# Kernel tuning notes

Hardware: AMD Instinct MI355X
Metric: run time of the kernel (lower is better)

The kernel has to match this reference:

```python
import jax, jax.numpy as jnp
import numpy as np

B, N_GLOBAL, D, E = 4096, 64, 256, 4
TPE = N_GLOBAL // E
EPS = 1e-5


def setup_inputs() -> dict:
    key = jax.random.key(0)
    ks = jax.random.split(key, 5)
    X_global = jax.random.normal(ks[0], (B, N_GLOBAL, D), dtype=jnp.float32)
    # per-expert deep MLP params: Linear(tpe*d -> d), Linear(d -> tpe*d)
    f = TPE * D
    W1 = jax.random.normal(ks[1], (E, f, D), dtype=jnp.float32) * (f ** -0.5)
    b1 = jax.random.normal(ks[2], (E, D), dtype=jnp.float32) * 0.01
    W2 = jax.random.normal(ks[3], (E, D, f), dtype=jnp.float32) * (D ** -0.5)
    b2 = jax.random.normal(ks[4], (E, f), dtype=jnp.float32) * 0.01
    gamma = jnp.ones((E, D), dtype=jnp.float32)
    beta = jnp.zeros((E, D), dtype=jnp.float32)
    return {"X_global": X_global, "W1": W1, "b1": b1, "W2": W2, "b2": b2,
            "gamma": gamma, "beta": beta}


def reference(X_global, W1, b1, W2, b2, gamma, beta):
    Bn, n_global, d = X_global.shape
    e = W1.shape[0]
    tpe = n_global // e
    scale = d ** -0.5
    # static partition: (B, E, tpe, d)
    Xp = X_global.reshape(Bn, e, tpe, d)
    # DOT-product self-attention per expert partition
    scores = jnp.einsum('bend,bemd->benm', Xp, Xp) * scale  # (B,E,tpe,tpe)
    X_dot = jnp.einsum('benm,bemd->bend', jax.nn.softmax(scores, axis=-1), Xp)
    # deep MLP on flattened partition
    Xf = Xp.reshape(Bn, e, tpe * d)
    h = jax.nn.relu(jnp.einsum('bef,efh->beh', Xf, W1) + b1[None])  # (B,E,d)
    X_deep = (jnp.einsum('beh,ehf->bef', h, W2) + b2[None]).reshape(Bn, e, tpe, d)
    # residual + LayerNorm over last dim (biased variance, eps=1e-5)
    Y = X_dot + X_deep + Xp
    mu = jnp.mean(Y, axis=-1, keepdims=True)
    var = jnp.mean(jnp.square(Y - mu), axis=-1, keepdims=True)
    Yn = (Y - mu) * jax.lax.rsqrt(var + EPS)
    Yn = Yn * gamma[None, :, None, :] + beta[None, :, None, :]
    return Yn.reshape(Bn, n_global, d)
```

## Files before the change

kernel.cpp:

```cpp
#include <hip/hip_runtime.h>


typedef __attribute__((ext_vector_type(4))) float f32x4;
typedef __bf16 bf16;
typedef __attribute__((ext_vector_type(8))) bf16 bf16x8;

#define DEV static __device__ __forceinline__

DEV f32x4 zero4() { return f32x4{0.f, 0.f, 0.f, 0.f}; }

DEV bf16x8 cvt8(const f32x4& a, const f32x4& b) {
  bf16x8 o;
  o[0] = (bf16)a.x; o[1] = (bf16)a.y; o[2] = (bf16)a.z; o[3] = (bf16)a.w;
  o[4] = (bf16)b.x; o[5] = (bf16)b.y; o[6] = (bf16)b.z; o[7] = (bf16)b.w;
  return o;
}

__global__ __launch_bounds__(256) void pack_w1(const float* __restrict__ W1,
                                               bf16* __restrict__ P) {
  const int e = blockIdx.z, kc = blockIdx.y;
  const int nf = blockIdx.x * 4 + (threadIdx.x >> 6);
  const int l = threadIdx.x & 63;
  const float* src = W1 + (size_t)e * 4096 * 256 +
                     (size_t)(kc * 32 + (l >> 4) * 8) * 256 + nf * 16 + (l & 15);
  bf16x8 o;
#pragma unroll
  for (int j = 0; j < 8; j++) o[j] = (bf16)src[(size_t)j * 256];
  *(bf16x8*)&P[(((size_t)e * 128 + kc) * 16 + nf) * 512 + l * 8] = o;
}

__global__ __launch_bounds__(256) void pack_w2(const float* __restrict__ W2,
                                               bf16* __restrict__ P) {
  const int e = blockIdx.z, t = blockIdx.y, kc = blockIdx.x;
  const int l = threadIdx.x & 63;
#pragma unroll
  for (int it = 0; it < 4; it++) {
    int nfl = it * 4 + (threadIdx.x >> 6);
    const float* src = W2 + (size_t)e * 256 * 4096 +
                       (size_t)(kc * 32 + (l >> 4) * 8) * 4096 + t * 256 +
                       nfl * 16 + (l & 15);
    bf16x8 o;
#pragma unroll
    for (int j = 0; j < 8; j++) o[j] = (bf16)src[(size_t)j * 4096];
    *(bf16x8*)&P[(((size_t)e * 256 + t * 16 + nfl) * 8 + kc) * 512 + l * 8] = o;
  }
}

__global__ __launch_bounds__(256) void fused_ag(
    const float* __restrict__ X, const bf16* __restrict__ W1P,
    const float* __restrict__ b1, float* __restrict__ Y0f,
    bf16* __restrict__ Y0b, bf16* __restrict__ HP, int useBf) {
  __shared__ __align__(16) bf16 S[4 * 4224];
  __shared__ __align__(16) bf16 Pl[4 * 512];
  const int tid = threadIdx.x, lane = tid & 63, w = tid >> 6;
  const int lr = lane & 15, g = lane >> 4;
  const int fid = blockIdx.x;
  const int e = (fid & 7) >> 1;
  const int m = ((fid >> 3) << 1) | (fid & 1);
  const int b0 = m * 32;

  {
    bf16* xt = &S[w * 4224];
    bf16* pl = &Pl[w * 512];
    for (int q = lane; q < 256; q += 64) {
      int row = q >> 4, cc = q & 15;
      pl[row * 32 + 16 + cc] = (bf16)0.f;
    }

    for (int q = 0; q < 8; q++) {
      const int bp = b0 + q * 4 + w;
      const size_t obase0 = (size_t)bp * 16384 + e * 4096;
      const float* Xb = X + obase0;

      xt[4096 + lane] = (bf16)0.f;

      bf16x8 af[8];
#pragma unroll
      for (int c = 0; c < 8; c++) {
        const float* qq = Xb + lr * 256 + c * 32 + g * 8;
        f32x4 v0 = *(const f32x4*)qq;
        f32x4 v1 = *(const f32x4*)(qq + 4);
        bf16x8 o = cvt8(v0, v1);
        af[c] = o;
#pragma unroll
        for (int j = 0; j < 8; j++)
          xt[(c * 32 + g * 8 + j) * 16 + lr] = o[j];
      }

      f32x4 s = zero4();
#pragma unroll
      for (int c = 0; c < 8; c++)
        s = __builtin_amdgcn_mfma_f32_16x16x32_bf16(af[c], af[c], s, 0, 0, 0);

      float pv[4];
#pragma unroll
      for (int r = 0; r < 4; r++) {
        float v = s[r] * 0.0625f;
        float mx = v;
#pragma unroll
        for (int mm = 1; mm < 16; mm <<= 1) mx = fmaxf(mx, __shfl_xor(mx, mm));
        float ev = __expf(v - mx);
        float sum = ev;
#pragma unroll
        for (int mm = 1; mm < 16; mm <<= 1) sum += __shfl_xor(sum, mm);
        pv[r] = ev / sum;
      }
#pragma unroll
      for (int r = 0; r < 4; r++) pl[(g * 4 + r) * 32 + lr] = (bf16)pv[r];
      bf16x8 pf = *(const bf16x8*)&pl[lr * 32 + g * 8];

      float yo[16][4];
#pragma unroll
      for (int nc = 0; nc < 16; nc++) {
        bf16x8 bfr = *(const bf16x8*)&xt[(nc * 16 + lr) * 16 + g * 8];
        f32x4 xd =
            __builtin_amdgcn_mfma_f32_16x16x32_bf16(pf, bfr, zero4(), 0, 0, 0);
#pragma unroll
        for (int r = 0; r < 4; r++)
          yo[nc][r] = xd[r] + (float)xt[(nc * 16 + lr) * 16 + g * 4 + r];
      }

#pragma unroll
      for (int nc = 0; nc < 16; nc++)
#pragma unroll
        for (int r = 0; r < 4; r++)
          xt[(g * 4 + r) * 264 + nc * 16 + lr] = (bf16)yo[nc][r];

      const int tok = lane >> 2, cc = lane & 3;
      if (useBf) {
#pragma unroll
        for (int i = 0; i < 8; i++) {
          int d0 = i * 32 + cc * 8;
          bf16x8 v = *(const bf16x8*)&xt[tok * 264 + d0];
          *(bf16x8*)&Y0b[obase0 + tok * 256 + d0] = v;
        }
      } else {
#pragma unroll
        for (int i = 0; i < 8; i++) {
          int d0 = i * 32 + cc * 8;
          bf16x8 v = *(const bf16x8*)&xt[tok * 264 + d0];
          f32x4 a, bb;
          a.x = (float)v[0]; a.y = (float)v[1];
          a.z = (float)v[2]; a.w = (float)v[3];
          bb.x = (float)v[4]; bb.y = (float)v[5];
          bb.z = (float)v[6]; bb.w = (float)v[7];
          *(f32x4*)&Y0f[obase0 + tok * 256 + d0] = a;
          *(f32x4*)&Y0f[obase0 + tok * 256 + d0 + 4] = bb;
        }
      }
    }
  }
  __syncthreads();

  {
    bf16* Ab0 = S;
    bf16* Ab1 = S + 4352;
    const int arow = tid >> 3, ak0 = (tid & 7) * 16;
    const size_t abase = (size_t)(b0 + arow) * 16384 + e * 4096 + ak0;
    const bf16* Wp = W1P + (size_t)e * 128 * 16 * 512;

    f32x4 acc[2][4];
#pragma unroll
    for (int i = 0; i < 2; i++)
#pragma unroll
      for (int j = 0; j < 4; j++) acc[i][j] = zero4();

    f32x4 p0, p1, p2, p3;
    {
      const float* q = X + abase;
      p0 = *(const f32x4*)q;       p1 = *(const f32x4*)(q + 4);
      p2 = *(const f32x4*)(q + 8); p3 = *(const f32x4*)(q + 12);
    }

    for (int kt = 0; kt < 32; kt++) {
      bf16* Ac = (kt & 1) ? Ab1 : Ab0;
      *(bf16x8*)&Ac[arow * 136 + ak0] = cvt8(p0, p1);
      *(bf16x8*)&Ac[arow * 136 + ak0 + 8] = cvt8(p2, p3);
      if (kt < 31) {
        const float* q = X + abase + (kt + 1) * 128;
        p0 = *(const f32x4*)q;       p1 = *(const f32x4*)(q + 4);
        p2 = *(const f32x4*)(q + 8); p3 = *(const f32x4*)(q + 12);
      }
      __syncthreads();
#pragma unroll
      for (int kki = 0; kki < 4; kki++) {
        const int kc = kt * 4 + kki;
        bf16x8 afr[2], bfr[4];
#pragma unroll
        for (int i = 0; i < 2; i++)
          afr[i] = *(const bf16x8*)&Ac[(i * 16 + lr) * 136 + kki * 32 + g * 8];
#pragma unroll
        for (int j = 0; j < 4; j++)
          bfr[j] = *(const bf16x8*)&Wp[(((size_t)kc) * 16 + w * 4 + j) * 512 +
                                       lane * 8];
#pragma unroll
        for (int i = 0; i < 2; i++)
#pragma unroll
          for (int j = 0; j < 4; j++)
            acc[i][j] = __builtin_amdgcn_mfma_f32_16x16x32_bf16(
                afr[i], bfr[j], acc[i][j], 0, 0, 0);
      }
      __syncthreads();
    }
#pragma unroll
    for (int j = 0; j < 4; j++) {
      const int col = w * 64 + j * 16 + lr;
      const float bv = b1[e * 256 + col];
      const int kc = col >> 5, lhi = (col >> 3) & 3, jj = col & 7;
#pragma unroll
      for (int i = 0; i < 2; i++) {
        const int mfg = m * 2 + i;
        bf16* dst = HP + (((size_t)e * 256 + mfg) * 8 + kc) * 512 + jj;
#pragma unroll
        for (int r = 0; r < 4; r++) {
          float v = fmaxf(acc[i][j][r] + bv, 0.f);
          dst[(lhi * 16 + g * 4 + r) * 8] = (bf16)v;
        }
      }
    }
  }
}

__global__ __launch_bounds__(512) void gemm2_kernel(
    const bf16* __restrict__ HP, const bf16* __restrict__ W2P,
    const float* __restrict__ b2, const float* __restrict__ gamma,
    const float* __restrict__ beta, const float* __restrict__ Y0f,
    const bf16* __restrict__ Y0b, int useBf, float* __restrict__ Out) {
  __shared__ __align__(16) bf16 T[64 * 264];
  const int fid = blockIdx.x;
  const int e = fid & 3;
  const int rr_ = fid >> 2;
  const int t = rr_ & 15;
  const int ms = rr_ >> 4;
  const int tid = threadIdx.x, lane = tid & 63, w = tid >> 6;
  const int lr = lane & 15, g = lane >> 4;
  const int erow = tid >> 3, ec = tid & 7;

  bf16x8 breg[2][8];
  {
    const bf16* Wp = W2P + (((size_t)e * 256 + t * 16 + w * 2) * 8) * 512 +
                     lane * 8;
#pragma unroll
    for (int nj = 0; nj < 2; nj++)
#pragma unroll
      for (int kc = 0; kc < 8; kc++)
        breg[nj][kc] = *(const bf16x8*)&Wp[(size_t)(nj * 8 + kc) * 512];
  }
  float b2v[2];
#pragma unroll
  for (int nj = 0; nj < 2; nj++)
    b2v[nj] = b2[e * 4096 + t * 256 + w * 32 + nj * 16 + lr];

  for (int it = 0; it < 2; it++) {
    const int mt = ms * 2 + it;
    const int b0 = mt * 64;
    const size_t ebase =
        (size_t)(b0 + erow) * 16384 + e * 4096 + t * 256 + ec * 32;

    bf16x8 y0r[4];
    if (useBf) {
#pragma unroll
      for (int u = 0; u < 4; u++)
        y0r[u] = *(const bf16x8*)&Y0b[ebase + u * 8];
    }

    const bf16* Ap = HP + (((size_t)e * 256 + mt * 4) * 8) * 512 + lane * 8;
    f32x4 acc[4][2];
#pragma unroll
    for (int mf = 0; mf < 4; mf++)
#pragma unroll
      for (int nj = 0; nj < 2; nj++) acc[mf][nj] = zero4();

    bf16x8 afr[4], afn[4];
#pragma unroll
    for (int mf = 0; mf < 4; mf++)
      afr[mf] = *(const bf16x8*)&Ap[(size_t)(mf * 8) * 512];
#pragma unroll
    for (int kc = 0; kc < 8; kc++) {
      if (kc < 7) {
#pragma unroll
        for (int mf = 0; mf < 4; mf++)
          afn[mf] = *(const bf16x8*)&Ap[(size_t)(mf * 8 + kc + 1) * 512];
      }
#pragma unroll
      for (int mf = 0; mf < 4; mf++)
#pragma unroll
        for (int nj = 0; nj < 2; nj++)
          acc[mf][nj] = __builtin_amdgcn_mfma_f32_16x16x32_bf16(
              afr[mf], breg[nj][kc], acc[mf][nj], 0, 0, 0);
#pragma unroll
      for (int mf = 0; mf < 4; mf++) afr[mf] = afn[mf];
    }

    __syncthreads();
#pragma unroll
    for (int mf = 0; mf < 4; mf++)
#pragma unroll
      for (int nj = 0; nj < 2; nj++)
#pragma unroll
        for (int r = 0; r < 4; r++)
          T[(mf * 16 + g * 4 + r) * 264 + w * 32 + nj * 16 + lr] =
              (bf16)(acc[mf][nj][r] + b2v[nj]);
    __syncthreads();

    float y[4][8];
    float s1 = 0.f, s2 = 0.f;
#pragma unroll
    for (int u = 0; u < 4; u++) {
      bf16x8 tv = *(const bf16x8*)&T[erow * 264 + ec * 32 + u * 8];
      if (useBf) {
#pragma unroll
        for (int u8 = 0; u8 < 8; u8++) {
          float v = (float)tv[u8] + (float)y0r[u][u8];
          y[u][u8] = v;
          s1 += v;
          s2 += v * v;
        }
      } else {
        f32x4 a = *(const f32x4*)&Y0f[ebase + u * 8];
        f32x4 bb = *(const f32x4*)&Y0f[ebase + u * 8 + 4];
#pragma unroll
        for (int u8 = 0; u8 < 8; u8++) {
          float v = (float)tv[u8] + (u8 < 4 ? a[u8] : bb[u8 - 4]);
          y[u][u8] = v;
          s1 += v;
          s2 += v * v;
        }
      }
    }
    s1 += __shfl_xor(s1, 1); s1 += __shfl_xor(s1, 2); s1 += __shfl_xor(s1, 4);
    s2 += __shfl_xor(s2, 1); s2 += __shfl_xor(s2, 2); s2 += __shfl_xor(s2, 4);
    const float mu = s1 * (1.f / 256.f);
    const float var = s2 * (1.f / 256.f) - mu * mu;
    const float rs = rsqrtf(var + 1e-5f);

#pragma unroll
    for (int u = 0; u < 4; u++) {
      const int col = ec * 32 + u * 8;
      f32x4 gv0 = *(const f32x4*)&gamma[e * 256 + col];
      f32x4 gv1 = *(const f32x4*)&gamma[e * 256 + col + 4];
      f32x4 bt0 = *(const f32x4*)&beta[e * 256 + col];
      f32x4 bt1 = *(const f32x4*)&beta[e * 256 + col + 4];
      f32x4 o0, o1;
#pragma unroll
      for (int u8 = 0; u8 < 4; u8++) {
        o0[u8] = (y[u][u8] - mu) * rs * gv0[u8] + bt0[u8];
        o1[u8] = (y[u][u8 + 4] - mu) * rs * gv1[u8] + bt1[u8];
      }
      *(f32x4*)&Out[ebase + u * 8] = o0;
      *(f32x4*)&Out[ebase + u * 8 + 4] = o1;
    }
  }
}

extern "C" void kernel_launch(void* const* d_in, const int* in_sizes, int n_in,
                              void* d_out, int out_size, void* d_ws, size_t ws_size,
                              hipStream_t stream) {
  const float* X     = (const float*)d_in[0];
  const float* W1    = (const float*)d_in[1];
  const float* b1    = (const float*)d_in[2];
  const float* W2    = (const float*)d_in[3];
  const float* b2    = (const float*)d_in[4];
  const float* gamma = (const float*)d_in[5];
  const float* beta  = (const float*)d_in[6];
  float* Out = (float*)d_out;

  const size_t MB8 = (size_t)4 * 1048576;
  bf16* W1P = (bf16*)d_ws;
  bf16* W2P = W1P + MB8;
  bf16* HP  = W2P + MB8;
  bf16* Y0b = HP + MB8;

  const size_t bigN = (size_t)4096 * 16384 * 2;
  const size_t base = 3 * (MB8 * 2);
  const int useBf = (ws_size >= base + bigN) ? 1 : 0;

  pack_w1<<<dim3(4, 128, 4), dim3(256), 0, stream>>>(W1, W1P);
  pack_w2<<<dim3(8, 16, 4), dim3(256), 0, stream>>>(W2, W2P);
  fused_ag<<<dim3(512), dim3(256), 0, stream>>>(X, W1P, b1, Out, Y0b, HP, useBf);
  gemm2_kernel<<<dim3(2048), dim3(512), 0, stream>>>(HP, W2P, b2, gamma, beta,
                                                     Out, Y0b, useBf, Out);
}
```

Baseline: 417.8 us.

## Double fused_ag waves, pad transposed LDS tile, retile GEMM1 with deeper K tiles

Raises fused_ag to 512 threads so the attention phase runs 8 waves over 4 iterations instead of 4 waves over 8. The transposed X tile in LDS now uses a row stride of 18 instead of 16, read with bf16x2 loads, to cut bank conflicts. GEMM1 is reorganised as a 2x4 wave grid, each wave holding one A fragment and 4 accumulators, with 256-wide K tiles and one barrier per tile instead of two. The trade-off is more LDS per block and fewer registers per wave, which could lower how many blocks fit on each CU.

```diff
diff --git a/kernel.cpp b/kernel.cpp
--- a/kernel.cpp
+++ b/kernel.cpp
@@ -4,6 +4,7 @@
 typedef __attribute__((ext_vector_type(4))) float f32x4;
 typedef __bf16 bf16;
 typedef __attribute__((ext_vector_type(8))) bf16 bf16x8;
+typedef __attribute__((ext_vector_type(2))) bf16 bf16x2;
 
 #define DEV static __device__ __forceinline__
 
@@ -46,12 +47,12 @@
   }
 }
 
-__global__ __launch_bounds__(256) void fused_ag(
+__global__ __launch_bounds__(512) void fused_ag(
     const float* __restrict__ X, const bf16* __restrict__ W1P,
     const float* __restrict__ b1, float* __restrict__ Y0f,
     bf16* __restrict__ Y0b, bf16* __restrict__ HP, int useBf) {
-  __shared__ __align__(16) bf16 S[4 * 4224];
-  __shared__ __align__(16) bf16 Pl[4 * 512];
+  __shared__ __align__(16) bf16 S[8 * 4608];
+  __shared__ __align__(16) bf16 Pl[8 * 512];
   const int tid = threadIdx.x, lane = tid & 63, w = tid >> 6;
   const int lr = lane & 15, g = lane >> 4;
   const int fid = blockIdx.x;
@@ -60,19 +61,18 @@
   const int b0 = m * 32;
 
   {
-    bf16* xt = &S[w * 4224];
+    bf16* xt = &S[w * 4608];
     bf16* pl = &Pl[w * 512];
     for (int q = lane; q < 256; q += 64) {
       int row = q >> 4, cc = q & 15;
       pl[row * 32 + 16 + cc] = (bf16)0.f;
     }
-
-    for (int q = 0; q < 8; q++) {
-      const int bp = b0 + q * 4 + w;
+    const int koff = (g & 1) * 8;
+
+    for (int q = 0; q < 4; q++) {
+      const int bp = b0 + q * 8 + w;
       const size_t obase0 = (size_t)bp * 16384 + e * 4096;
       const float* Xb = X + obase0;
-
-      xt[4096 + lane] = (bf16)0.f;
 
       bf16x8 af[8];
 #pragma unroll
@@ -84,7 +84,7 @@
         af[c] = o;
 #pragma unroll
         for (int j = 0; j < 8; j++)
-          xt[(c * 32 + g * 8 + j) * 16 + lr] = o[j];
+          xt[(c * 32 + g * 8 + j) * 18 + lr] = o[j];
       }
 
       f32x4 s = zero4();
@@ -112,12 +112,22 @@
       float yo[16][4];
 #pragma unroll
       for (int nc = 0; nc < 16; nc++) {
-        bf16x8 bfr = *(const bf16x8*)&xt[(nc * 16 + lr) * 16 + g * 8];
+        const bf16* rowp = &xt[(nc * 16 + lr) * 18];
+        bf16x8 bfr;
+#pragma unroll
+        for (int h = 0; h < 4; h++) {
+          bf16x2 tv = *(const bf16x2*)&rowp[koff + h * 2];
+          bfr[2 * h] = tv[0];
+          bfr[2 * h + 1] = tv[1];
+        }
         f32x4 xd =
             __builtin_amdgcn_mfma_f32_16x16x32_bf16(pf, bfr, zero4(), 0, 0, 0);
-#pragma unroll
-        for (int r = 0; r < 4; r++)
-          yo[nc][r] = xd[r] + (float)xt[(nc * 16 + lr) * 16 + g * 4 + r];
+        bf16x2 r01 = *(const bf16x2*)&rowp[g * 4];
+        bf16x2 r23 = *(const bf16x2*)&rowp[g * 4 + 2];
+        yo[nc][0] = xd[0] + (float)r01[0];
+        yo[nc][1] = xd[1] + (float)r01[1];
+        yo[nc][2] = xd[2] + (float)r23[0];
+        yo[nc][3] = xd[3] + (float)r23[1];
       }
 
 #pragma unroll
@@ -154,16 +164,15 @@
 
   {
     bf16* Ab0 = S;
-    bf16* Ab1 = S + 4352;
-    const int arow = tid >> 3, ak0 = (tid & 7) * 16;
+    bf16* Ab1 = S + 8448;
+    const int wm = w >> 2, wn = w & 3;
+    const int arow = tid >> 4, ak0 = (tid & 15) * 16;
     const size_t abase = (size_t)(b0 + arow) * 16384 + e * 4096 + ak0;
     const bf16* Wp = W1P + (size_t)e * 128 * 16 * 512;
 
-    f32x4 acc[2][4];
-#pragma unroll
-    for (int i = 0; i < 2; i++)
-#pragma unroll
-      for (int j = 0; j < 4; j++) acc[i][j] = zero4();
+    f32x4 acc[4];
+#pragma unroll
+    for (int j = 0; j < 4; j++) acc[j] = zero4();
 
     f32x4 p0, p1, p2, p3;
     {
@@ -172,50 +181,43 @@
       p2 = *(const f32x4*)(q + 8); p3 = *(const f32x4*)(q + 12);
     }
 
-    for (int kt = 0; kt < 32; kt++) {
+    for (int kt = 0; kt < 16; kt++) {
       bf16* Ac = (kt & 1) ? Ab1 : Ab0;
-      *(bf16x8*)&Ac[arow * 136 + ak0] = cvt8(p0, p1);
-      *(bf16x8*)&Ac[arow * 136 + ak0 + 8] = cvt8(p2, p3);
-      if (kt < 31) {
-        const float* q = X + abase + (kt + 1) * 128;
+      *(bf16x8*)&Ac[arow * 264 + ak0] = cvt8(p0, p1);
+      *(bf16x8*)&Ac[arow * 264 + ak0 + 8] = cvt8(p2, p3);
+      if (kt < 15) {
+        const float* q = X + abase + (kt + 1) * 256;
         p0 = *(const f32x4*)q;       p1 = *(const f32x4*)(q + 4);
         p2 = *(const f32x4*)(q + 8); p3 = *(const f32x4*)(q + 12);
       }
       __syncthreads();
 #pragma unroll
-      for (int kki = 0; kki < 4; kki++) {
-        const int kc = kt * 4 + kki;
-        bf16x8 afr[2], bfr[4];
-#pragma unroll
-        for (int i = 0; i < 2; i++)
-          afr[i] = *(const bf16x8*)&Ac[(i * 16 + lr) * 136 + kki * 32 + g * 8];
+      for (int kki = 0; kki < 8; kki++) {
+        const int kc = kt * 8 + kki;
+        bf16x8 a =
+            *(const bf16x8*)&Ac[(wm * 16 + lr) * 264 + kki * 32 + g * 8];
+        bf16x8 bfr[4];
 #pragma unroll
         for (int j = 0; j < 4; j++)
-          bfr[j] = *(const bf16x8*)&Wp[(((size_t)kc) * 16 + w * 4 + j) * 512 +
+          bfr[j] = *(const bf16x8*)&Wp[(((size_t)kc) * 16 + wn * 4 + j) * 512 +
                                        lane * 8];
 #pragma unroll
-        for (int i = 0; i < 2; i++)
-#pragma unroll
-          for (int j = 0; j < 4; j++)
-            acc[i][j] = __builtin_amdgcn_mfma_f32_16x16x32_bf16(
-                afr[i], bfr[j], acc[i][j], 0, 0, 0);
-      }
-      __syncthreads();
+        for (int j = 0; j < 4; j++)
+          acc[j] = __builtin_amdgcn_mfma_f32_16x16x32_bf16(a, bfr[j], acc[j],
+                                                           0, 0, 0);
+      }
     }
 #pragma unroll
     for (int j = 0; j < 4; j++) {
-      const int col = w * 64 + j * 16 + lr;
+      const int col = wn * 64 + j * 16 + lr;
       const float bv = b1[e * 256 + col];
       const int kc = col >> 5, lhi = (col >> 3) & 3, jj = col & 7;
-#pragma unroll
-      for (int i = 0; i < 2; i++) {
-        const int mfg = m * 2 + i;
-        bf16* dst = HP + (((size_t)e * 256 + mfg) * 8 + kc) * 512 + jj;
-#pragma unroll
-        for (int r = 0; r < 4; r++) {
-          float v = fmaxf(acc[i][j][r] + bv, 0.f);
-          dst[(lhi * 16 + g * 4 + r) * 8] = (bf16)v;
-        }
+      const int mfg = m * 2 + wm;
+      bf16* dst = HP + (((size_t)e * 256 + mfg) * 8 + kc) * 512 + jj;
+#pragma unroll
+      for (int r = 0; r < 4; r++) {
+        float v = fmaxf(acc[j][r] + bv, 0.f);
+        dst[(lhi * 16 + g * 4 + r) * 8] = (bf16)v;
       }
     }
   }
@@ -377,7 +379,7 @@
 
   pack_w1<<<dim3(4, 128, 4), dim3(256), 0, stream>>>(W1, W1P);
   pack_w2<<<dim3(8, 16, 4), dim3(256), 0, stream>>>(W2, W2P);
-  fused_ag<<<dim3(512), dim3(256), 0, stream>>>(X, W1P, b1, Out, Y0b, HP, useBf);
+  fused_ag<<<dim3(512), dim3(512), 0, stream>>>(X, W1P, b1, Out, Y0b, HP, useBf);
   gemm2_kernel<<<dim3(2048), dim3(512), 0, stream>>>(HP, W2P, b2, gamma, beta,
                                                      Out, Y0b, useBf, Out);
 }
```

New measurement: 460.1 us. 10.1% more time.

## Prefetch next X tile into registers, pad LDS stride, drop loop barrier

Applied to the files above, without the earlier changes.

The attention stage in fused_ag now loads the next batch row's X tile into registers while the current tile's softmax and P·X MMAs run. The goal is to hide global-load latency behind compute. The transposed LDS tile gains a row stride of 18 to reduce bank conflicts, and reads switch to bf16x2. Per-iteration zeroing of the K padding is dropped: the upper K half reads duplicated data that the zeroed P columns cancel. A __syncthreads at the end of the W1 GEMM k-loop is removed; this is only correct if the shared A buffer is not overwritten before all waves finish reading it. Register pressure also rises from the 16 prefetched f32x4 values.

```diff
diff --git a/kernel.cpp b/kernel.cpp
--- a/kernel.cpp
+++ b/kernel.cpp
@@ -4,6 +4,7 @@
 typedef __attribute__((ext_vector_type(4))) float f32x4;
 typedef __bf16 bf16;
 typedef __attribute__((ext_vector_type(8))) bf16 bf16x8;
+typedef __attribute__((ext_vector_type(2))) bf16 bf16x2;
 
 #define DEV static __device__ __forceinline__
 
@@ -50,7 +51,7 @@
     const float* __restrict__ X, const bf16* __restrict__ W1P,
     const float* __restrict__ b1, float* __restrict__ Y0f,
     bf16* __restrict__ Y0b, bf16* __restrict__ HP, int useBf) {
-  __shared__ __align__(16) bf16 S[4 * 4224];
+  __shared__ __align__(16) bf16 S[4 * 4608];
   __shared__ __align__(16) bf16 Pl[4 * 512];
   const int tid = threadIdx.x, lane = tid & 63, w = tid >> 6;
   const int lr = lane & 15, g = lane >> 4;
@@ -60,37 +61,53 @@
   const int b0 = m * 32;
 
   {
-    bf16* xt = &S[w * 4224];
+    bf16* xt = &S[w * 4608];
     bf16* pl = &Pl[w * 512];
     for (int q = lane; q < 256; q += 64) {
       int row = q >> 4, cc = q & 15;
       pl[row * 32 + 16 + cc] = (bf16)0.f;
     }
+    const int koff = (g & 1) * 8;
+
+    f32x4 raw[16];
+    {
+      const float* Xb = X + (size_t)(b0 + w) * 16384 + e * 4096;
+#pragma unroll
+      for (int c = 0; c < 8; c++) {
+        const float* qq = Xb + lr * 256 + c * 32 + g * 8;
+        raw[2 * c] = *(const f32x4*)qq;
+        raw[2 * c + 1] = *(const f32x4*)(qq + 4);
+      }
+    }
 
     for (int q = 0; q < 8; q++) {
       const int bp = b0 + q * 4 + w;
       const size_t obase0 = (size_t)bp * 16384 + e * 4096;
-      const float* Xb = X + obase0;
-
-      xt[4096 + lane] = (bf16)0.f;
 
       bf16x8 af[8];
 #pragma unroll
       for (int c = 0; c < 8; c++) {
-        const float* qq = Xb + lr * 256 + c * 32 + g * 8;
-        f32x4 v0 = *(const f32x4*)qq;
-        f32x4 v1 = *(const f32x4*)(qq + 4);
-        bf16x8 o = cvt8(v0, v1);
+        bf16x8 o = cvt8(raw[2 * c], raw[2 * c + 1]);
         af[c] = o;
 #pragma unroll
         for (int j = 0; j < 8; j++)
-          xt[(c * 32 + g * 8 + j) * 16 + lr] = o[j];
+          xt[(c * 32 + g * 8 + j) * 18 + lr] = o[j];
       }
 
       f32x4 s = zero4();
 #pragma unroll
       for (int c = 0; c < 8; c++)
         s = __builtin_amdgcn_mfma_f32_16x16x32_bf16(af[c], af[c], s, 0, 0, 0);
+
+      if (q < 7) {
+        const float* Xb = X + (size_t)(bp + 4) * 16384 + e * 4096;
+#pragma unroll
+        for (int c = 0; c < 8; c++) {
+          const float* qq = Xb + lr * 256 + c * 32 + g * 8;
+          raw[2 * c] = *(const f32x4*)qq;
+          raw[2 * c + 1] = *(const f32x4*)(qq + 4);
+        }
+      }
 
       float pv[4];
 #pragma unroll
@@ -112,12 +129,22 @@
       float yo[16][4];
 #pragma unroll
       for (int nc = 0; nc < 16; nc++) {
-        bf16x8 bfr = *(const bf16x8*)&xt[(nc * 16 + lr) * 16 + g * 8];
+        const bf16* rowp = &xt[(nc * 16 + lr) * 18];
+        bf16x8 bfr;
+#pragma unroll
+        for (int h = 0; h < 4; h++) {
+          bf16x2 tv = *(const bf16x2*)&rowp[koff + h * 2];
+          bfr[2 * h] = tv[0];
+          bfr[2 * h + 1] = tv[1];
+        }
         f32x4 xd =
             __builtin_amdgcn_mfma_f32_16x16x32_bf16(pf, bfr, zero4(), 0, 0, 0);
-#pragma unroll
-        for (int r = 0; r < 4; r++)
-          yo[nc][r] = xd[r] + (float)xt[(nc * 16 + lr) * 16 + g * 4 + r];
+        bf16x2 r01 = *(const bf16x2*)&rowp[g * 4];
+        bf16x2 r23 = *(const bf16x2*)&rowp[g * 4 + 2];
+        yo[nc][0] = xd[0] + (float)r01[0];
+        yo[nc][1] = xd[1] + (float)r01[1];
+        yo[nc][2] = xd[2] + (float)r23[0];
+        yo[nc][3] = xd[3] + (float)r23[1];
       }
 
 #pragma unroll
@@ -200,7 +227,6 @@
             acc[i][j] = __builtin_amdgcn_mfma_f32_16x16x32_bf16(
                 afr[i], bfr[j], acc[i][j], 0, 0, 0);
       }
-      __syncthreads();
     }
 #pragma unroll
     for (int j = 0; j < 4; j++) {
```

Result: faster. 405.6 us (-2.9%).
